# Performance work log

Measured on AMD Instinct MI355X. Metric: run time of the kernel, lower is better.

The kernel has to match this reference:

```python
import jax, jax.numpy as jnp
import numpy as np

DOMAIN_MIN, DOMAIN_MAX = -1.0, 1.0
N, D_IN, D_OUT, K = 1024, 128, 128, 8


def setup_inputs() -> dict:
    key = jax.random.key(0)
    k1, k2, k3 = jax.random.split(key, 3)
    x = jax.random.uniform(k1, (N, D_IN), dtype=jnp.float32,
                           minval=DOMAIN_MIN, maxval=DOMAIN_MAX)
    # Per-edge spline knot values: near-identity init plus small noise.
    base = jnp.linspace(DOMAIN_MIN, DOMAIN_MAX, K, dtype=jnp.float32)
    coeffs = base[None, None, :] + 0.1 * jax.random.normal(
        k2, (D_OUT, D_IN, K), dtype=jnp.float32)
    weights = jax.random.normal(k3, (D_OUT, D_IN), dtype=jnp.float32) * np.sqrt(2.0 / D_IN)
    bias = jnp.zeros((D_OUT,), dtype=jnp.float32)
    return {"x": x, "coeffs": coeffs, "weights": weights, "bias": bias}


def _spline_all_edges(x, coeffs):
    """Evaluate every edge's cubic (Catmull-Rom) spline at its input.
    x: [N, d_in]; coeffs: [d_out, d_in, K] knot values on uniform knots in [-1,1].
    Returns s: [N, d_in, d_out]."""
    K_ = coeffs.shape[-1]
    h = (DOMAIN_MAX - DOMAIN_MIN) / (K_ - 1)
    xc = jnp.clip(x, DOMAIN_MIN, DOMAIN_MAX)
    t = (xc - DOMAIN_MIN) / h                      # [N, d_in], in [0, K-1]
    idx = jnp.clip(jnp.floor(t).astype(jnp.int32), 0, K_ - 2)
    u = t - idx                                    # local coord in [0,1]
    i0 = jnp.clip(idx - 1, 0, K_ - 1)
    i1 = idx
    i2 = idx + 1
    i3 = jnp.clip(idx + 2, 0, K_ - 1)
    ct = jnp.transpose(coeffs, (1, 2, 0))          # [d_in, K, d_out]
    jar = jnp.arange(ct.shape[0])[None, :]          # [1, d_in]
    p0 = ct[jar, i0]                               # [N, d_in, d_out]
    p1 = ct[jar, i1]
    p2 = ct[jar, i2]
    p3 = ct[jar, i3]
    u2 = u * u
    u3 = u2 * u
    b0 = 0.5 * (-u3 + 2.0 * u2 - u)
    b1 = 0.5 * (3.0 * u3 - 5.0 * u2 + 2.0)
    b2 = 0.5 * (-3.0 * u3 + 4.0 * u2 + u)
    b3 = 0.5 * (u3 - u2)
    return (b0[..., None] * p0 + b1[..., None] * p1 +
            b2[..., None] * p2 + b3[..., None] * p3)


def reference(x, coeffs, weights, bias):
    # h_i(x) = sum_j w_ij * s_ij(x_j) + b_i
    s = _spline_all_edges(x, coeffs)               # [N, d_in, d_out]
    return jnp.einsum('njo,oj->no', s, weights) + bias[None, :]
```

## Files before the change

kernel.cpp:

```cpp
#include <hip/hip_runtime.h>
#include <hip/hip_bf16.h>
#include <stdint.h>


#define DIN 128
#define DOUT 128
#define KTOT 1024
#define MT 16
#define PADW 1032

typedef unsigned int u32;
typedef unsigned short u16;
typedef __attribute__((ext_vector_type(8))) short bf16x8;
typedef __attribute__((ext_vector_type(4))) float f32x4;

__device__ __forceinline__ u16 f2b(float f) {
    union { __hip_bfloat16 h; u16 u; } c;
    c.h = __float2bfloat16(f);
    return c.u;
}

__global__ __launch_bounds__(256) void kan_mfma(
    const float* __restrict__ x, const float* __restrict__ coeffs,
    const float* __restrict__ weights, const float* __restrict__ bias,
    float* __restrict__ out)
{
    __shared__ __align__(16) u16 sA[MT * PADW];
    __shared__ float sC[4 * 256];

    const int tid  = threadIdx.x;
    const int wave = tid >> 6;
    const int lane = tid & 63;
    const int n0 = blockIdx.x * MT;
    const int og = blockIdx.y * 32;

    #pragma unroll
    for (int it = 0; it < 8; ++it) {
        const int z = tid + it * 256;
        const int row = z >> 7, c16 = z & 127;
        *(uint4*)(sA + row * PADW + c16 * 8) = uint4{0u, 0u, 0u, 0u};
    }
    __syncthreads();

    #pragma unroll
    for (int it = 0; it < 8; ++it) {
        const int task = tid + it * 256;
        const int row = task >> 7;
        const int j = task & 127;
        float xv = x[(n0 + row) * DIN + j];
        xv = fminf(fmaxf(xv, -1.0f), 1.0f);
        const float t = (xv + 1.0f) * 3.5f;
        int idx = (int)t; idx = idx > 6 ? 6 : idx;
        const float u = t - (float)idx;
        const float u2 = u * u, u3 = u2 * u;
        const float b0 = 0.5f * (-u3 + 2.0f * u2 - u);
        const float b1 = 0.5f * (3.0f * u3 - 5.0f * u2 + 2.0f);
        const float b2 = 0.5f * (-3.0f * u3 + 4.0f * u2 + u);
        const float b3 = 0.5f * (u3 - u2);
        u16* r = sA + row * PADW + j * 8;
        const int i0 = idx > 0 ? idx - 1 : 0;
        const int i3 = idx < 6 ? idx + 2 : 7;
        r[idx]     = f2b(b1);
        r[idx + 1] = f2b(b2);
        r[i0]      = f2b(idx == 0 ? b0 + b1 : b0);
        r[i3]      = f2b(idx == 6 ? b2 + b3 : b3);
    }
    __syncthreads();

    const int ot = wave & 1;
    const int kh = wave >> 1;
    const int mo = lane & 15;
    const int q  = lane >> 4;

    const int orow = og + ot * 16 + mo;
    const float* cp = coeffs + orow * KTOT + kh * 512 + q * 8;
    const float* wp = weights + orow * DIN + kh * 64 + q;
    const u16*   ap = sA + mo * PADW + kh * 512 + q * 8;

    f32x4 acc = {0.0f, 0.0f, 0.0f, 0.0f};
    #pragma unroll 4
    for (int s = 0; s < 16; ++s) {
        bf16x8 af = *(const bf16x8*)(ap + s * 32);
        const float4 c0 = *(const float4*)(cp + s * 32);
        const float4 c1 = *(const float4*)(cp + s * 32 + 4);
        const float wv = wp[s * 4];
        bf16x8 bfr;
        bfr[0] = (short)f2b(c0.x * wv); bfr[1] = (short)f2b(c0.y * wv);
        bfr[2] = (short)f2b(c0.z * wv); bfr[3] = (short)f2b(c0.w * wv);
        bfr[4] = (short)f2b(c1.x * wv); bfr[5] = (short)f2b(c1.y * wv);
        bfr[6] = (short)f2b(c1.z * wv); bfr[7] = (short)f2b(c1.w * wv);
        acc = __builtin_amdgcn_mfma_f32_16x16x32_bf16(af, bfr, acc, 0, 0, 0);
    }

    #pragma unroll
    for (int r = 0; r < 4; ++r)
        sC[wave * 256 + (q * 4 + r) * 16 + mo] = acc[r];
    __syncthreads();

    #pragma unroll
    for (int t2 = 0; t2 < 2; ++t2) {
        const int e = tid + t2 * 256;
        const int tile = e >> 8;
        const int idx = e & 255;
        const int row = idx >> 4, col = idx & 15;
        float v = sC[tile * 256 + idx] + sC[(tile + 2) * 256 + idx];
        const int oc = og + tile * 16 + col;
        out[(n0 + row) * DOUT + oc] = v + bias[oc];
    }
}

extern "C" void kernel_launch(void* const* d_in, const int* in_sizes, int n_in,
                              void* d_out, int out_size, void* d_ws, size_t ws_size,
                              hipStream_t stream) {
    const float* x       = (const float*)d_in[0];
    const float* coeffs  = (const float*)d_in[1];
    const float* weights = (const float*)d_in[2];
    const float* bias    = (const float*)d_in[3];
    float* out = (float*)d_out;
    const int N = in_sizes[0] / DIN;
    dim3 grid(N / MT, DOUT / 32);
    kan_mfma<<<grid, 256, 0, stream>>>(x, coeffs, weights, bias, out);
}
```

Measured before the change: 65.12 us.

## Double block size to 512 threads, split K four ways, write basis rows vectorized

The block grows from 4 to 8 waves. Each wave now covers a quarter of the K dimension (8 MFMA steps instead of 16), and the four partial results per tile are summed through shared memory. The separate shared-memory zeroing pass and its barrier are removed. Each thread instead builds its 8 basis weights in registers and stores them as one 16-byte write. The aim is more parallelism to hide the global coeff loads and fewer LDS writes and barriers, at the cost of a larger cross-wave reduction and more threads per block.

After: 66.93 us. 1.03x slower.

```diff
diff --git a/kernel.cpp b/kernel.cpp
--- a/kernel.cpp
+++ b/kernel.cpp
@@ -14,19 +14,21 @@
 typedef __attribute__((ext_vector_type(8))) short bf16x8;
 typedef __attribute__((ext_vector_type(4))) float f32x4;
 
+union H8 { u16 s[8]; uint4 v; };
+
 __device__ __forceinline__ u16 f2b(float f) {
     union { __hip_bfloat16 h; u16 u; } c;
     c.h = __float2bfloat16(f);
     return c.u;
 }
 
-__global__ __launch_bounds__(256) void kan_mfma(
+__global__ __launch_bounds__(512) void kan_mfma(
     const float* __restrict__ x, const float* __restrict__ coeffs,
     const float* __restrict__ weights, const float* __restrict__ bias,
     float* __restrict__ out)
 {
     __shared__ __align__(16) u16 sA[MT * PADW];
-    __shared__ float sC[4 * 256];
+    __shared__ float sC[8 * 256];
 
     const int tid  = threadIdx.x;
     const int wave = tid >> 6;
@@ -35,16 +37,8 @@
     const int og = blockIdx.y * 32;
 
     #pragma unroll
-    for (int it = 0; it < 8; ++it) {
-        const int z = tid + it * 256;
-        const int row = z >> 7, c16 = z & 127;
-        *(uint4*)(sA + row * PADW + c16 * 8) = uint4{0u, 0u, 0u, 0u};
-    }
-    __syncthreads();
-
-    #pragma unroll
-    for (int it = 0; it < 8; ++it) {
-        const int task = tid + it * 256;
+    for (int it = 0; it < 4; ++it) {
+        const int task = tid + it * 512;
         const int row = task >> 7;
         const int j = task & 127;
         float xv = x[(n0 + row) * DIN + j];
@@ -57,29 +51,32 @@
         const float b1 = 0.5f * (3.0f * u3 - 5.0f * u2 + 2.0f);
         const float b2 = 0.5f * (-3.0f * u3 + 4.0f * u2 + u);
         const float b3 = 0.5f * (u3 - u2);
-        u16* r = sA + row * PADW + j * 8;
+        float r[8];
+        #pragma unroll
+        for (int k = 0; k < 8; ++k) r[k] = 0.0f;
         const int i0 = idx > 0 ? idx - 1 : 0;
         const int i3 = idx < 6 ? idx + 2 : 7;
-        r[idx]     = f2b(b1);
-        r[idx + 1] = f2b(b2);
-        r[i0]      = f2b(idx == 0 ? b0 + b1 : b0);
-        r[i3]      = f2b(idx == 6 ? b2 + b3 : b3);
+        r[i0] += b0; r[idx] += b1; r[idx + 1] += b2; r[i3] += b3;
+        H8 h;
+        #pragma unroll
+        for (int k = 0; k < 8; ++k) h.s[k] = f2b(r[k]);
+        *(uint4*)(sA + row * PADW + j * 8) = h.v;
     }
     __syncthreads();
 
     const int ot = wave & 1;
-    const int kh = wave >> 1;
+    const int kq = wave >> 1;
     const int mo = lane & 15;
     const int q  = lane >> 4;
 
     const int orow = og + ot * 16 + mo;
-    const float* cp = coeffs + orow * KTOT + kh * 512 + q * 8;
-    const float* wp = weights + orow * DIN + kh * 64 + q;
-    const u16*   ap = sA + mo * PADW + kh * 512 + q * 8;
+    const float* cp = coeffs + orow * KTOT + kq * 256 + q * 8;
+    const float* wp = weights + orow * DIN + kq * 32 + q;
+    const u16*   ap = sA + mo * PADW + kq * 256 + q * 8;
 
     f32x4 acc = {0.0f, 0.0f, 0.0f, 0.0f};
-    #pragma unroll 4
-    for (int s = 0; s < 16; ++s) {
+    #pragma unroll
+    for (int s = 0; s < 8; ++s) {
         bf16x8 af = *(const bf16x8*)(ap + s * 32);
         const float4 c0 = *(const float4*)(cp + s * 32);
         const float4 c1 = *(const float4*)(cp + s * 32 + 4);
@@ -97,13 +94,12 @@
         sC[wave * 256 + (q * 4 + r) * 16 + mo] = acc[r];
     __syncthreads();
 
-    #pragma unroll
-    for (int t2 = 0; t2 < 2; ++t2) {
-        const int e = tid + t2 * 256;
-        const int tile = e >> 8;
-        const int idx = e & 255;
+    {
+        const int tile = tid >> 8;
+        const int idx = tid & 255;
         const int row = idx >> 4, col = idx & 15;
-        float v = sC[tile * 256 + idx] + sC[(tile + 2) * 256 + idx];
+        float v = sC[(0 + tile) * 256 + idx] + sC[(2 + tile) * 256 + idx]
+                + sC[(4 + tile) * 256 + idx] + sC[(6 + tile) * 256 + idx];
         const int oc = og + tile * 16 + col;
         out[(n0 + row) * DOUT + oc] = v + bias[oc];
     }
@@ -119,5 +115,5 @@
     float* out = (float*)d_out;
     const int N = in_sizes[0] / DIN;
     dim3 grid(N / MT, DOUT / 32);
-    kan_mfma<<<grid, 256, 0, stream>>>(x, coeffs, weights, bias, out);
+    kan_mfma<<<grid, 512, 0, stream>>>(x, coeffs, weights, bias, out);
 }
```
